# Kernel tuning notes

Measured on AMD Instinct MI355X. Metric: run time of the kernel, lower is better.

## Reference

```python
import jax, jax.numpy as jnp
import numpy as np

RADIUS = 0.1
MAX_NEIGHBORS = 64


def setup_inputs() -> dict:
    key0 = jax.random.key(0)
    k1, k2 = jax.random.split(key0)
    query = jax.random.uniform(k1, (4, 2048, 3), dtype=jnp.float32)
    key = jax.random.uniform(k2, (4, 8192, 3), dtype=jnp.float32)
    return {"query": query, "key": key}


def reference(query, key):
    # PointNet++-style ball query: for each query point, the indices of the
    # first MAX_NEIGHBORS key points (in key order) with squared distance
    # < RADIUS^2; remaining slots are padded with the first found neighbor
    # index (0 if no neighbor exists, matching zero-initialized CUDA output).
    B, N1, _ = query.shape
    N2 = key.shape[1]
    K = MAX_NEIGHBORS

    # [B, N1, N2] squared pairwise distances
    d2 = jnp.sum((query[:, :, None, :] - key[:, None, :, :]) ** 2, axis=-1)
    within = d2 < jnp.float32(RADIUS) ** 2  # [B, N1, N2] bool

    # slot each valid neighbor lands in (in key-index order)
    pos = jnp.cumsum(within.astype(jnp.int32), axis=-1) - 1  # [B, N1, N2]
    take = within & (pos < K)
    slot = jnp.where(take, pos, K)  # invalid entries routed to dummy slot K

    n2_idx = jnp.broadcast_to(jnp.arange(N2, dtype=jnp.int32), (B, N1, N2))
    b_idx = jnp.arange(B)[:, None, None]
    n1_idx = jnp.arange(N1)[None, :, None]

    out = jnp.full((B, N1, K + 1), -1, dtype=jnp.int32)
    # slots < K are unique per (b, n1); duplicates only at dummy slot K
    out = out.at[b_idx, n1_idx, slot].set(n2_idx)
    out = out[..., :K]  # drop dummy slot

    # pad empty slots with index of first in-radius neighbor (0 if none)
    first = jnp.argmax(within, axis=-1).astype(jnp.int32)  # [B, N1]
    out = jnp.where(out < 0, first[..., None], out)
    return out
```

## Files before the change

### kernel.cpp

```cpp
#include <hip/hip_runtime.h>


constexpr int   K    = 64;
constexpr float R2   = 0.01f;
constexpr int   B    = 4;
constexpr int   N1   = 2048;
constexpr int   N2   = 8192;
constexpr int   GC   = 5;
constexpr int   NCELL = GC * GC * GC;
constexpr float INVCELL = 5.0f;
constexpr int   SUBS_PER_B = 32;
constexpr int   SUBS       = B * SUBS_PER_B;

constexpr size_t SORTED_BYTES = (size_t)B * N2 * 16;
constexpr size_t CS_BYTES     = (size_t)B * (NCELL + 1) * 4;
constexpr size_t WS_NEEDED    = SORTED_BYTES + CS_BYTES;

__device__ __forceinline__ int cell_of(float v) {
    int c = (int)(v * INVCELL);
    return c < 0 ? 0 : (c > GC - 1 ? GC - 1 : c);
}

__global__ __launch_bounds__(256) void build_kernel(
    const float* __restrict__ key,
    int* __restrict__ cell_start,
    float4* __restrict__ sorted)
{
    __shared__ int h_tot[NCELL];
    __shared__ int h_pre[NCELL];
    __shared__ int sbuf[128];
    __shared__ int cursor[NCELL];

    const int k = blockIdx.x;
    const int b = k >> 5;
    const int s = k & 31;
    const int t = threadIdx.x;

    if (t < NCELL) { h_tot[t] = 0; h_pre[t] = 0; }
    __syncthreads();

    const float* kb = key + (size_t)b * N2 * 3;
    float mx = 0.f, my = 0.f, mz = 0.f;
    int mycell = 0;
    for (int i = 0; i < SUBS_PER_B; ++i) {
        const int j = i * 256 + t;
        const float x = kb[j * 3 + 0];
        const float y = kb[j * 3 + 1];
        const float z = kb[j * 3 + 2];
        const int c = (cell_of(x) * GC + cell_of(y)) * GC + cell_of(z);
        atomicAdd(&h_tot[c], 1);
        if (i < s) atomicAdd(&h_pre[c], 1);
        if (i == s) { mx = x; my = y; mz = z; mycell = c; }
    }
    __syncthreads();

    const int total = (t < NCELL) ? h_tot[t] : 0;
    if (t < 128) sbuf[t] = total;
    __syncthreads();
    for (int off = 1; off < 128; off <<= 1) {
        int v = 0;
        if (t < 128 && t >= off) v = sbuf[t - off];
        __syncthreads();
        if (t < 128) sbuf[t] += v;
        __syncthreads();
    }
    if (t < NCELL) {
        const int excl = sbuf[t] - total;
        cursor[t] = excl + h_pre[t];
        if (s == 0) {
            cell_start[b * (NCELL + 1) + t + 1] = sbuf[t];
            if (t == 0) cell_start[b * (NCELL + 1)] = 0;
        }
    }
    __syncthreads();

    const int pos = atomicAdd(&cursor[mycell], 1);
    float4 v;
    v.x = mx; v.y = my; v.z = mz; v.w = __int_as_float(s * 256 + t);
    sorted[(size_t)b * N2 + pos] = v;
}

__global__ __launch_bounds__(256) void ballquery_grid_kernel(
    const float* __restrict__ query,
    const float4* __restrict__ sorted,
    const int* __restrict__ cell_start,
    int* __restrict__ out)
{
    __shared__ unsigned int bm[4 * 256];

    const int lane = threadIdx.x & 63;
    const int wv   = threadIdx.x >> 6;
    const int q    = blockIdx.x * 4 + wv;
    const int b    = q >> 11;

    const float qx = query[q * 3 + 0];
    const float qy = query[q * 3 + 1];
    const float qz = query[q * 3 + 2];

    const float ux = qx * INVCELL, uy = qy * INVCELL, uz = qz * INVCELL;
    const int cx = cell_of(qx), cy = cell_of(qy), cz = cell_of(qz);
    const int nx = (ux - cx < 0.5f) ? cx - 1 : cx + 1;
    const int ny = (uy - cy < 0.5f) ? cy - 1 : cy + 1;
    const int nz = (uz - cz < 0.5f) ? cz - 1 : cz + 1;
    const int xlo = max(0, min(cx, nx)), xhi = min(GC - 1, max(cx, nx));
    const int ylo = max(0, min(cy, ny)), yhi = min(GC - 1, max(cy, ny));
    const int zlo = max(0, min(cz, nz)), zhi = min(GC - 1, max(cz, nz));

    unsigned int* wbm = bm + wv * 256;
    uint4 zz; zz.x = zz.y = zz.z = zz.w = 0u;
    ((uint4*)wbm)[lane] = zz;

    const int*    cs = cell_start + b * (NCELL + 1);
    const float4* sb = sorted + (size_t)b * N2;

    for (int xx = xlo; xx <= xhi; ++xx) {
        for (int yy = ylo; yy <= yhi; ++yy) {
            const int colz = (xx * GC + yy) * GC;
            const int s = cs[colz + zlo];
            const int e = cs[colz + zhi + 1];
            for (int t0 = s; t0 < e; t0 += 64) {
                const int i = t0 + lane;
                const float4 kv = sb[min(i, e - 1)];
                const float dx = kv.x - qx;
                const float dy = kv.y - qy;
                const float dz = kv.z - qz;
                const bool within = (i < e) && (dx * dx + dy * dy + dz * dz < R2);
                if (within) {
                    const int id = __float_as_int(kv.w);
                    atomicOr(&wbm[id >> 5], 1u << (id & 31));
                }
            }
        }
    }

    const uint4 w = ((const uint4*)wbm)[lane];
    const int c = __popc(w.x) + __popc(w.y) + __popc(w.z) + __popc(w.w);

    int x = c;
    #pragma unroll
    for (int off = 1; off < 64; off <<= 1) {
        int y = __shfl_up(x, off);
        if (lane >= off) x += y;
    }
    const int base = x - c;
    const int cnt  = __shfl(x, 63);

    int fs;
    if      (w.x) fs = __builtin_ctz(w.x);
    else if (w.y) fs = 32 + __builtin_ctz(w.y);
    else if (w.z) fs = 64 + __builtin_ctz(w.z);
    else if (w.w) fs = 96 + __builtin_ctz(w.w);
    else          fs = 0;
    int myfirst = c ? (lane << 7) + fs : 0x7fffffff;
    #pragma unroll
    for (int off = 32; off; off >>= 1)
        myfirst = min(myfirst, __shfl_xor(myfirst, off));
    const int firstIdx = (cnt == 0) ? 0 : myfirst;

    int* op = out + q * K;
    int slot = base;
    unsigned int wr[4] = {w.x, w.y, w.z, w.w};
    #pragma unroll
    for (int r = 0; r < 4; ++r) {
        unsigned int m = wr[r];
        const int bb = (lane << 7) + (r << 5);
        while (m) {
            const int bp = __builtin_ctz(m);
            m &= m - 1;
            if (slot < K) op[slot] = bb + bp;
            ++slot;
        }
    }

    const int kpad = cnt < K ? cnt : K;
    const int s2 = kpad + lane;
    if (s2 < K) op[s2] = firstIdx;
}

__global__ __launch_bounds__(256) void ballquery_bruteforce_kernel(
    const float* __restrict__ query, const float* __restrict__ key,
    int* __restrict__ out)
{
    const int lane = threadIdx.x & 63;
    const int q = blockIdx.x * 4 + (threadIdx.x >> 6);
    const int b = q >> 11;
    const float qx = query[q * 3], qy = query[q * 3 + 1], qz = query[q * 3 + 2];
    const float* kb = key + (size_t)b * N2 * 3;
    int* op = out + (size_t)q * K;
    int count = 0, first = 0;
    bool have_first = false;
    const unsigned long long lane_mask_lt = (lane == 0) ? 0ull : (~0ull >> (64 - lane));
    for (int c = 0; c < N2 / 64; ++c) {
        if (count >= K) break;
        const int j = (c << 6) + lane;
        const float* kp = kb + j * 3;
        const float dx = kp[0] - qx, dy = kp[1] - qy, dz = kp[2] - qz;
        const bool within = dx * dx + dy * dy + dz * dz < R2;
        const unsigned long long mask = __ballot(within);
        if (mask) {
            if (!have_first) { first = (c << 6) + __builtin_ctzll(mask); have_first = true; }
            if (within) {
                const int slot = count + __popcll(mask & lane_mask_lt);
                if (slot < K) op[slot] = j;
            }
            count += __popcll(mask);
        }
    }
    const int cnt = count < K ? count : K;
    if (cnt + lane < K) op[cnt + lane] = first;
}

extern "C" void kernel_launch(void* const* d_in, const int* in_sizes, int n_in,
                              void* d_out, int out_size, void* d_ws, size_t ws_size,
                              hipStream_t stream) {
    const float* query = (const float*)d_in[0];
    const float* key   = (const float*)d_in[1];
    int* out = (int*)d_out;

    if (ws_size < WS_NEEDED) {
        ballquery_bruteforce_kernel<<<(B * N1) / 4, 256, 0, stream>>>(query, key, out);
        return;
    }

    float4* sorted     = (float4*)d_ws;
    int*    cell_start = (int*)((char*)d_ws + SORTED_BYTES);

    build_kernel<<<SUBS, 256, 0, stream>>>(key, cell_start, sorted);
    ballquery_grid_kernel<<<(B * N1) / 4, 256, 0, stream>>>(query, sorted, cell_start, out);
}
```

Baseline: 76.09 us.

## Replace grid-based ball query with two-queries-per-wave brute-force scan

Result: slower. 96.16 us (+26.4%).

```diff
diff --git a/kernel.cpp b/kernel.cpp
--- a/kernel.cpp
+++ b/kernel.cpp
@@ -1,213 +1,79 @@
 #include <hip/hip_runtime.h>
 
 
-constexpr int   K    = 64;
-constexpr float R2   = 0.01f;
-constexpr int   B    = 4;
-constexpr int   N1   = 2048;
-constexpr int   N2   = 8192;
-constexpr int   GC   = 5;
-constexpr int   NCELL = GC * GC * GC;
-constexpr float INVCELL = 5.0f;
-constexpr int   SUBS_PER_B = 32;
-constexpr int   SUBS       = B * SUBS_PER_B;
+constexpr int   K  = 64;
+constexpr float R2 = 0.01f;
+constexpr int   B  = 4;
+constexpr int   N1 = 2048;
+constexpr int   N2 = 8192;
 
-constexpr size_t SORTED_BYTES = (size_t)B * N2 * 16;
-constexpr size_t CS_BYTES     = (size_t)B * (NCELL + 1) * 4;
-constexpr size_t WS_NEEDED    = SORTED_BYTES + CS_BYTES;
+__global__ __launch_bounds__(256) void bq_brute2_kernel(
+    const float* __restrict__ query,
+    const float* __restrict__ key,
+    int* __restrict__ out)
+{
+    const int lane = threadIdx.x & 63;
+    const int w    = blockIdx.x * 4 + (threadIdx.x >> 6);
+    const int q0   = w * 2;
+    const int q1   = q0 + 1;
+    const int b    = q0 >> 11;
 
-__device__ __forceinline__ int cell_of(float v) {
-    int c = (int)(v * INVCELL);
-    return c < 0 ? 0 : (c > GC - 1 ? GC - 1 : c);
-}
-
-__global__ __launch_bounds__(256) void build_kernel(
-    const float* __restrict__ key,
-    int* __restrict__ cell_start,
-    float4* __restrict__ sorted)
-{
-    __shared__ int h_tot[NCELL];
-    __shared__ int h_pre[NCELL];
-    __shared__ int sbuf[128];
-    __shared__ int cursor[NCELL];
-
-    const int k = blockIdx.x;
-    const int b = k >> 5;
-    const int s = k & 31;
-    const int t = threadIdx.x;
-
-    if (t < NCELL) { h_tot[t] = 0; h_pre[t] = 0; }
-    __syncthreads();
+    const float qx0 = query[q0 * 3 + 0];
+    const float qy0 = query[q0 * 3 + 1];
+    const float qz0 = query[q0 * 3 + 2];
+    const float qx1 = query[q1 * 3 + 0];
+    const float qy1 = query[q1 * 3 + 1];
+    const float qz1 = query[q1 * 3 + 2];
 
     const float* kb = key + (size_t)b * N2 * 3;
-    float mx = 0.f, my = 0.f, mz = 0.f;
-    int mycell = 0;
-    for (int i = 0; i < SUBS_PER_B; ++i) {
-        const int j = i * 256 + t;
+    const unsigned long long below =
+        (lane == 0) ? 0ull : (~0ull >> (64 - lane));
+
+    int cnt0 = 0, cnt1 = 0, f0 = -1, f1 = -1;
+    int* op0 = out + (size_t)q0 * K;
+    int* op1 = out + (size_t)q1 * K;
+
+    #pragma unroll 4
+    for (int c = 0; c < N2 / 64; ++c) {
+        const int j = (c << 6) + lane;
         const float x = kb[j * 3 + 0];
         const float y = kb[j * 3 + 1];
         const float z = kb[j * 3 + 2];
-        const int c = (cell_of(x) * GC + cell_of(y)) * GC + cell_of(z);
-        atomicAdd(&h_tot[c], 1);
-        if (i < s) atomicAdd(&h_pre[c], 1);
-        if (i == s) { mx = x; my = y; mz = z; mycell = c; }
-    }
-    __syncthreads();
 
-    const int total = (t < NCELL) ? h_tot[t] : 0;
-    if (t < 128) sbuf[t] = total;
-    __syncthreads();
-    for (int off = 1; off < 128; off <<= 1) {
-        int v = 0;
-        if (t < 128 && t >= off) v = sbuf[t - off];
-        __syncthreads();
-        if (t < 128) sbuf[t] += v;
-        __syncthreads();
-    }
-    if (t < NCELL) {
-        const int excl = sbuf[t] - total;
-        cursor[t] = excl + h_pre[t];
-        if (s == 0) {
-            cell_start[b * (NCELL + 1) + t + 1] = sbuf[t];
-            if (t == 0) cell_start[b * (NCELL + 1)] = 0;
+        {
+            const float dx = x - qx0, dy = y - qy0, dz = z - qz0;
+            const bool within = dx * dx + dy * dy + dz * dz < R2;
+            const unsigned long long m = __ballot(within);
+            if (m) {
+                if (f0 < 0) f0 = (c << 6) + __builtin_ctzll(m);
+                if (within) {
+                    const int slot = cnt0 + __popcll(m & below);
+                    if (slot < K) op0[slot] = j;
+                }
+                cnt0 += __popcll(m);
+            }
         }
-    }
-    __syncthreads();
-
-    const int pos = atomicAdd(&cursor[mycell], 1);
-    float4 v;
-    v.x = mx; v.y = my; v.z = mz; v.w = __int_as_float(s * 256 + t);
-    sorted[(size_t)b * N2 + pos] = v;
-}
-
-__global__ __launch_bounds__(256) void ballquery_grid_kernel(
-    const float* __restrict__ query,
-    const float4* __restrict__ sorted,
-    const int* __restrict__ cell_start,
-    int* __restrict__ out)
-{
-    __shared__ unsigned int bm[4 * 256];
-
-    const int lane = threadIdx.x & 63;
-    const int wv   = threadIdx.x >> 6;
-    const int q    = blockIdx.x * 4 + wv;
-    const int b    = q >> 11;
-
-    const float qx = query[q * 3 + 0];
-    const float qy = query[q * 3 + 1];
-    const float qz = query[q * 3 + 2];
-
-    const float ux = qx * INVCELL, uy = qy * INVCELL, uz = qz * INVCELL;
-    const int cx = cell_of(qx), cy = cell_of(qy), cz = cell_of(qz);
-    const int nx = (ux - cx < 0.5f) ? cx - 1 : cx + 1;
-    const int ny = (uy - cy < 0.5f) ? cy - 1 : cy + 1;
-    const int nz = (uz - cz < 0.5f) ? cz - 1 : cz + 1;
-    const int xlo = max(0, min(cx, nx)), xhi = min(GC - 1, max(cx, nx));
-    const int ylo = max(0, min(cy, ny)), yhi = min(GC - 1, max(cy, ny));
-    const int zlo = max(0, min(cz, nz)), zhi = min(GC - 1, max(cz, nz));
-
-    unsigned int* wbm = bm + wv * 256;
-    uint4 zz; zz.x = zz.y = zz.z = zz.w = 0u;
-    ((uint4*)wbm)[lane] = zz;
-
-    const int*    cs = cell_start + b * (NCELL + 1);
-    const float4* sb = sorted + (size_t)b * N2;
-
-    for (int xx = xlo; xx <= xhi; ++xx) {
-        for (int yy = ylo; yy <= yhi; ++yy) {
-            const int colz = (xx * GC + yy) * GC;
-            const int s = cs[colz + zlo];
-            const int e = cs[colz + zhi + 1];
-            for (int t0 = s; t0 < e; t0 += 64) {
-                const int i = t0 + lane;
-                const float4 kv = sb[min(i, e - 1)];
-                const float dx = kv.x - qx;
-                const float dy = kv.y - qy;
-                const float dz = kv.z - qz;
-                const bool within = (i < e) && (dx * dx + dy * dy + dz * dz < R2);
+        {
+            const float dx = x - qx1, dy = y - qy1, dz = z - qz1;
+            const bool within = dx * dx + dy * dy + dz * dz < R2;
+            const unsigned long long m = __ballot(within);
+            if (m) {
+                if (f1 < 0) f1 = (c << 6) + __builtin_ctzll(m);
                 if (within) {
-                    const int id = __float_as_int(kv.w);
-                    atomicOr(&wbm[id >> 5], 1u << (id & 31));
+                    const int slot = cnt1 + __popcll(m & below);
+                    if (slot < K) op1[slot] = j;
                 }
+                cnt1 += __popcll(m);
             }
         }
     }
 
-    const uint4 w = ((const uint4*)wbm)[lane];
-    const int c = __popc(w.x) + __popc(w.y) + __popc(w.z) + __popc(w.w);
-
-    int x = c;
-    #pragma unroll
-    for (int off = 1; off < 64; off <<= 1) {
-        int y = __shfl_up(x, off);
-        if (lane >= off) x += y;
-    }
-    const int base = x - c;
-    const int cnt  = __shfl(x, 63);
-
-    int fs;
-    if      (w.x) fs = __builtin_ctz(w.x);
-    else if (w.y) fs = 32 + __builtin_ctz(w.y);
-    else if (w.z) fs = 64 + __builtin_ctz(w.z);
-    else if (w.w) fs = 96 + __builtin_ctz(w.w);
-    else          fs = 0;
-    int myfirst = c ? (lane << 7) + fs : 0x7fffffff;
-    #pragma unroll
-    for (int off = 32; off; off >>= 1)
-        myfirst = min(myfirst, __shfl_xor(myfirst, off));
-    const int firstIdx = (cnt == 0) ? 0 : myfirst;
-
-    int* op = out + q * K;
-    int slot = base;
-    unsigned int wr[4] = {w.x, w.y, w.z, w.w};
-    #pragma unroll
-    for (int r = 0; r < 4; ++r) {
-        unsigned int m = wr[r];
-        const int bb = (lane << 7) + (r << 5);
-        while (m) {
-            const int bp = __builtin_ctz(m);
-            m &= m - 1;
-            if (slot < K) op[slot] = bb + bp;
-            ++slot;
-        }
-    }
-
-    const int kpad = cnt < K ? cnt : K;
-    const int s2 = kpad + lane;
-    if (s2 < K) op[s2] = firstIdx;
-}
-
-__global__ __launch_bounds__(256) void ballquery_bruteforce_kernel(
-    const float* __restrict__ query, const float* __restrict__ key,
-    int* __restrict__ out)
-{
-    const int lane = threadIdx.x & 63;
-    const int q = blockIdx.x * 4 + (threadIdx.x >> 6);
-    const int b = q >> 11;
-    const float qx = query[q * 3], qy = query[q * 3 + 1], qz = query[q * 3 + 2];
-    const float* kb = key + (size_t)b * N2 * 3;
-    int* op = out + (size_t)q * K;
-    int count = 0, first = 0;
-    bool have_first = false;
-    const unsigned long long lane_mask_lt = (lane == 0) ? 0ull : (~0ull >> (64 - lane));
-    for (int c = 0; c < N2 / 64; ++c) {
-        if (count >= K) break;
-        const int j = (c << 6) + lane;
-        const float* kp = kb + j * 3;
-        const float dx = kp[0] - qx, dy = kp[1] - qy, dz = kp[2] - qz;
-        const bool within = dx * dx + dy * dy + dz * dz < R2;
-        const unsigned long long mask = __ballot(within);
-        if (mask) {
-            if (!have_first) { first = (c << 6) + __builtin_ctzll(mask); have_first = true; }
-            if (within) {
-                const int slot = count + __popcll(mask & lane_mask_lt);
-                if (slot < K) op[slot] = j;
-            }
-            count += __popcll(mask);
-        }
-    }
-    const int cnt = count < K ? count : K;
-    if (cnt + lane < K) op[cnt + lane] = first;
+    const int first0 = (f0 < 0) ? 0 : f0;
+    const int first1 = (f1 < 0) ? 0 : f1;
+    const int c0 = cnt0 < K ? cnt0 : K;
+    const int c1 = cnt1 < K ? cnt1 : K;
+    if (c0 + lane < K) op0[c0 + lane] = first0;
+    if (c1 + lane < K) op1[c1 + lane] = first1;
 }
 
 extern "C" void kernel_launch(void* const* d_in, const int* in_sizes, int n_in,
@@ -216,15 +82,7 @@
     const float* query = (const float*)d_in[0];
     const float* key   = (const float*)d_in[1];
     int* out = (int*)d_out;
+    (void)d_ws; (void)ws_size;
 
-    if (ws_size < WS_NEEDED) {
-        ballquery_bruteforce_kernel<<<(B * N1) / 4, 256, 0, stream>>>(query, key, out);
-        return;
-    }
-
-    float4* sorted     = (float4*)d_ws;
-    int*    cell_start = (int*)((char*)d_ws + SORTED_BYTES);
-
-    build_kernel<<<SUBS, 256, 0, stream>>>(key, cell_start, sorted);
-    ballquery_grid_kernel<<<(B * N1) / 4, 256, 0, stream>>>(query, sorted, cell_start, out);
+    bq_brute2_kernel<<<(B * N1) / 8, 256, 0, stream>>>(query, key, out);
 }
```
